# Optimization experiments

Hardware: AMD Instinct MI355X
Metric: run time of the kernel (lower is better)

## Reference

```python
import jax, jax.numpy as jnp
import numpy as np
from jax import lax

DF = 64        # forcing_size: number of teacher-forced latent dims
TF_ALPHA = 0.2 # generalized teacher forcing interpolation weight


def setup_inputs() -> dict:
    key = jax.random.key(0)
    ks = jax.random.split(key, 8)
    B, T, dx, dz, dh, S = 256, 1024, 64, 256, 1024, 16
    x_gt = jax.random.normal(ks[0], (B, T, dx), dtype=jnp.float32)
    subject = jax.random.randint(ks[1], (B,), 0, S, dtype=jnp.int32)
    obs_matrix = jax.random.normal(ks[2], (dz, dx), dtype=jnp.float32) * 0.1
    A_table = jax.random.uniform(ks[3], (S, dz), dtype=jnp.float32) * 0.9
    W1_table = jax.random.normal(ks[4], (S, dz, dh), dtype=jnp.float32) * 0.02
    W2_table = jax.random.normal(ks[5], (S, dh, dz), dtype=jnp.float32) * 0.02
    h1_table = jax.random.normal(ks[6], (S, dz), dtype=jnp.float32) * 0.02
    h2_table = jax.random.normal(ks[7], (S, dh), dtype=jnp.float32) * 0.02
    return {"x_gt": x_gt, "subject": subject, "obs_matrix": obs_matrix,
            "A_table": A_table, "W1_table": W1_table, "W2_table": W2_table,
            "h1_table": h1_table, "h2_table": h2_table}


def reference(x_gt, subject, obs_matrix, A_table, W1_table, W2_table, h1_table, h2_table):
    B, T, dx = x_gt.shape
    dz = obs_matrix.shape[0]
    # encode: x @ pinv(obs_matrix) -> (B, T, dz)
    forcing = x_gt @ jnp.linalg.pinv(obs_matrix)
    # gather per-sample parameters by subject id
    A = A_table[subject]    # (B, dz)
    W1 = W1_table[subject]  # (B, dz, dh)
    W2 = W2_table[subject]  # (B, dh, dz)
    h1 = h1_table[subject]  # (B, dz)
    h2 = h2_table[subject]  # (B, dh)

    z0 = jnp.zeros((B, dz), dtype=x_gt.dtype)
    z0 = z0.at[:, :DF].set(forcing[:, 0, :DF])

    def step(z, f_t):
        # generalized teacher forcing on first DF dims
        z = z.at[:, :DF].set(TF_ALPHA * f_t[:, :DF] + (1.0 - TF_ALPHA) * z[:, :DF])
        # vanilla shPLRNN step: A*z + W1 @ relu(W2 @ z + h2) + h1
        hidden = jax.nn.relu(jnp.einsum('bhz,bz->bh', W2, z) + h2)
        z = A * z + jnp.einsum('bzh,bh->bz', W1, hidden) + h1
        return z, z

    _, Z = lax.scan(step, z0, jnp.transpose(forcing, (1, 0, 2)))  # Z: (T, B, dz)
    # decode: (B, T, dz) @ (dz, dx)
    return jnp.transpose(Z, (1, 0, 2)) @ obs_matrix
```

## Files before the change

kernel.cpp:

```cpp
#include <hip/hip_runtime.h>


typedef _Float16 f16;
typedef _Float16 f16x8 __attribute__((ext_vector_type(8)));
typedef float f32x4 __attribute__((ext_vector_type(4)));

#define TSTEPS 1024

#define WS_C     0ul
#define WS_ZG    16384ul
#define WS_HIDG  802816ul
#define WS_ORDER 2375680ul
#define WS_CNT   2376704ul
#define WS_OFFS  2376768ul
#define WS_CTR   2376832ul
#define WS_XCC   2378880ul
#define WS_FLAG  2379392ul
#define WS_NEED  2381440ul

#define SM_ZPK   0
#define SM_ZPRE  26880
#define SM_ZSL   33792
#define SM_TBUF  39936
#define SM_AH    53760
#define SM_ORD   54016
#define SM_SIZE  54208

__device__ __forceinline__ unsigned pack2f16(float x, float y) {
    union { f16 h[2]; unsigned u; } v;
    v.h[0] = (f16)x; v.h[1] = (f16)y;
    return v.u;
}

__device__ __forceinline__ void group_barrier(int* ctr, int target,
                                              int* flg, int j, int gen,
                                              bool light) {
    __syncthreads();
    if (light) {
        if (threadIdx.x < 64) {
            if (threadIdx.x == 0)
                *(volatile int*)(flg + j) = gen;
            volatile const int* fp = (volatile const int*)(flg + (threadIdx.x & 7));
            for (;;) {
                asm volatile("buffer_inv" ::: "memory");
                int v = *fp;
                if (__all(v >= gen)) break;
                __builtin_amdgcn_s_sleep(1);
            }
            asm volatile("buffer_inv" ::: "memory");
        }
        __syncthreads();
        return;
    }
    if (threadIdx.x == 0) {
        __builtin_amdgcn_fence(__ATOMIC_RELEASE, "agent");
        __hip_atomic_fetch_add(ctr, 1, __ATOMIC_RELAXED, __HIP_MEMORY_SCOPE_AGENT);
        while (__hip_atomic_load(ctr, __ATOMIC_RELAXED, __HIP_MEMORY_SCOPE_AGENT) < target)
            __builtin_amdgcn_s_sleep(1);
        __builtin_amdgcn_fence(__ATOMIC_ACQUIRE, "agent");
    }
    __syncthreads();
}

__global__ __launch_bounds__(256) void prep_kernel(const float* __restrict__ M,
                                                   float* __restrict__ C) {
    __shared__ float aug[64 * 132];
    __shared__ float fac[64];
    int tid = threadIdx.x;
    {
        int i = tid >> 2;
        int j0 = (tid & 3) * 16;
        float acc[16];
        #pragma unroll
        for (int e = 0; e < 16; ++e) acc[e] = 0.f;
        for (int r = 0; r < 256; ++r) {
            float mi = M[r*64 + i];
            #pragma unroll
            for (int e = 0; e < 16; ++e) acc[e] += mi * M[r*64 + j0 + e];
        }
        #pragma unroll
        for (int e = 0; e < 16; ++e) aug[i*132 + j0 + e] = acc[e];
    }
    for (int idx = tid; idx < 4096; idx += 256) {
        int x = idx >> 6, c = idx & 63;
        aug[x*132 + 64 + c] = M[c*64 + x];
    }
    __syncthreads();
    for (int p = 0; p < 64; ++p) {
        float piv = aug[p*132 + p];
        __syncthreads();
        if (tid < 128) aug[p*132 + tid] /= piv;
        __syncthreads();
        if (tid < 64) fac[tid] = aug[tid*132 + p];
        __syncthreads();
        for (int idx = tid; idx < 8192; idx += 256) {
            int r = idx >> 7, c = idx & 127;
            if (r != p) aug[r*132 + c] -= fac[r] * aug[p*132 + c];
        }
        __syncthreads();
    }
    for (int idx = tid; idx < 4096; idx += 256) {
        int x = idx >> 6, c = idx & 63;
        C[x*64 + c] = aug[x*132 + 64 + c];
    }
}

__global__ __launch_bounds__(256) void forcing_kernel(const float* __restrict__ x,
        const float* __restrict__ C, float* __restrict__ fout) {
    __shared__ float xs[64 * 68];
    __shared__ float Cs[64 * 64];
    int tid = threadIdx.x;
    for (int i = tid; i < 1024; i += 256)
        ((float4*)Cs)[i] = ((const float4*)C)[i];
    long r0 = (long)blockIdx.x * 64;
    int b  = (int)(r0 >> 10);
    int t0 = (int)(r0 & 1023);
    const float4* xb = (const float4*)(x + ((long)b * 1024 + t0) * 64);
    for (int i = tid; i < 1024; i += 256) {
        float4 v = xb[i];
        int row = i >> 4, col = (i & 15) * 4;
        *(float4*)&xs[row*68 + col] = v;
    }
    __syncthreads();
    int row = tid >> 2, cg = (tid & 3) * 16;
    float acc[16];
    #pragma unroll
    for (int e = 0; e < 16; ++e) acc[e] = 0.f;
    for (int k = 0; k < 64; ++k) {
        float xv = xs[row*68 + k];
        const float* cr = &Cs[k*64 + cg];
        #pragma unroll
        for (int e = 0; e < 16; ++e) acc[e] += xv * cr[e];
    }
    float4* dst = (float4*)(fout + ((size_t)b*1024 + t0 + row)*64 + cg);
    #pragma unroll
    for (int e = 0; e < 4; ++e) {
        float4 v; v.x = acc[4*e]; v.y = acc[4*e+1]; v.z = acc[4*e+2]; v.w = acc[4*e+3];
        dst[e] = v;
    }
}

__global__ __launch_bounds__(256) void group_kernel(const int* __restrict__ subject,
        int* order, int* cnt, int* offs, int* ctr, int* flag) {
    __shared__ int lc[16], lo[16], cur[16];
    int tid = threadIdx.x;
    if (tid < 16) { lc[tid] = 0; cur[tid] = 0; }
    __syncthreads();
    int s = subject[tid];
    atomicAdd(&lc[s], 1);
    __syncthreads();
    if (tid == 0) { int a = 0; for (int i = 0; i < 16; ++i) { lo[i] = a; a += lc[i]; } }
    __syncthreads();
    int pos = lo[s] + atomicAdd(&cur[s], 1);
    order[pos] = tid;
    if (tid < 16) {
        cnt[tid] = lc[tid]; offs[tid] = lo[tid];
        ctr[tid*32] = 0;
        ctr[tid*32 + 16] = 0;
        #pragma unroll
        for (int k = 0; k < 8; ++k) flag[tid*32 + k] = 0;
    }
}

template<int NT>
__device__ __forceinline__ void run_group(int s, int j, int Bs, int off,
    const float* __restrict__ W1t, const float* __restrict__ W2t,
    const float* __restrict__ At,  const float* __restrict__ h1t,
    const float* __restrict__ h2t, const float* __restrict__ Mt,
    float* __restrict__ zg, f16* __restrict__ hidg,
    const int* __restrict__ order, int* ctr, int* flg,
    float* out, char* sm, bool light)
{
    f16*   zpk   = (f16*)(sm + SM_ZPK);
    f16*   zpre  = (f16*)(sm + SM_ZPRE);
    float* zsl   = (float*)(sm + SM_ZSL);
    f16*   tbuf  = (f16*)(sm + SM_TBUF);
    float* ah    = (float*)(sm + SM_AH);
    int*   ordl  = (int*)(sm + SM_ORD);
    float* red   = (float*)(sm + SM_ZPK);

    const int tid  = threadIdx.x;
    const int w    = tid >> 6;
    const int lane = tid & 63;
    const int q    = lane >> 4;
    const int li   = lane & 15;

    float* zgs = zg + (size_t)s * (48*256);
    char*  hgs = (char*)hidg + (size_t)s * (48*1024*2);

    if (tid < 48) ordl[tid] = (tid < Bs) ? order[off + tid] : 0;
    if (tid >= 64 && tid < 96)  ah[tid-64]      = At [s*256 + 32*j + (tid-64)];
    if (tid >= 96 && tid < 128) ah[tid-96+32]   = h1t[s*256 + 32*j + (tid-96)];
    __syncthreads();

    f16x8 w2f[2][8], w1f[2][8], mfr[8];
    float h2v[2][4];
    const f32x4 zero4 = {0.f, 0.f, 0.f, 0.f};
    #pragma unroll
    for (int m = 0; m < 2; ++m) {
        const float* src = W2t + (size_t)s*262144 + (size_t)(128*j + (2*w+m)*16 + li)*256;
        #pragma unroll
        for (int kt = 0; kt < 8; ++kt) {
            int k0 = kt*32 + q*8;
            #pragma unroll
            for (int e = 0; e < 8; ++e) w2f[m][kt][e] = (f16)src[k0+e];
        }
    }
    #pragma unroll
    for (int m = 0; m < 2; ++m) {
        const float* src = W1t + (size_t)s*262144 + (size_t)(32*j + m*16 + li)*1024;
        #pragma unroll
        for (int kt = 0; kt < 8; ++kt) {
            int k0 = (8*w + kt)*32 + q*8;
            #pragma unroll
            for (int e = 0; e < 8; ++e) w1f[m][kt][e] = (f16)src[k0+e];
        }
    }
    #pragma unroll
    for (int kt = 0; kt < 8; ++kt)
        #pragma unroll
        for (int e = 0; e < 8; ++e)
            mfr[kt][e] = (f16)Mt[(kt*32 + q*8 + e)*64 + 16*w + li];
    #pragma unroll
    for (int m = 0; m < 2; ++m)
        #pragma unroll
        for (int r = 0; r < 4; ++r)
            h2v[m][r] = h2t[s*1024 + 128*j + (2*w+m)*16 + q*4 + r];

    for (int idx = tid; idx < NT*512; idx += 256) {
        int n = idx >> 5, zdl = idx & 31;
        int zd = 32*j + zdl;
        float v = 0.f;
        if (zd < 64 && n < Bs) v = out[(size_t)ordl[n]*65536 + zd];
        zgs[n*256 + zd] = v;
    }
    int gen = 1;
    group_barrier(ctr, 8*gen, flg, j, gen, light);

    for (int t = 0; t <= TSTEPS; ++t) {
        {
            int half = tid >> 7;
            int kk = (tid & 127) * 2;
            int kl = kk - 32*j;
            #pragma unroll
            for (int i = 0; i < NT*8; ++i) {
                int n = i*2 + half;
                float zx = 0.f, zy = 0.f;
                if (n < Bs) {
                    float2 zz = *(const float2*)&zgs[n*256 + kk];
                    zx = zz.x; zy = zz.y;
                }
                float px = zx, py = zy;
                if (kk < 64) {
                    ((unsigned*)zpre)[n*36 + (kk>>1)] = pack2f16(zx, zy);
                    if (t < TSTEPS && n < Bs) {
                        float2 fv = *(const float2*)&out[((size_t)ordl[n]*1024 + t)*64 + kk];
                        px = 0.2f*fv.x + 0.8f*zx;
                        py = 0.2f*fv.y + 0.8f*zy;
                    }
                }
                ((unsigned*)zpk)[n*140 + (kk>>1)] = pack2f16(px, py);
                if (kl >= 0 && kl < 32) {
                    float2 pv; pv.x = px; pv.y = py;
                    *(float2*)&zsl[n*32 + kl] = pv;
                }
            }
        }
        __syncthreads();

        if (t > 0 && j < NT) {
            f32x4 dacc = zero4;
            #pragma unroll
            for (int kt = 0; kt < 8; ++kt) {
                f16x8 af;
                if (kt < 2) af = *(const f16x8*)&zpre[(16*j + li)*72 + kt*32 + q*8];
                else        af = *(const f16x8*)&zpk [(16*j + li)*280 + kt*32 + q*8];
                dacc = __builtin_amdgcn_mfma_f32_16x16x32_f16(af, mfr[kt], dacc, 0, 0, 0);
            }
            #pragma unroll
            for (int r = 0; r < 4; ++r) {
                int n = 16*j + q*4 + r;
                if (n < Bs)
                    out[((size_t)ordl[n]*TSTEPS + (t-1))*64 + 16*w + li] = dacc[r];
            }
        }
        if (t == TSTEPS) break;

        {
            f32x4 acc[2][NT];
            #pragma unroll
            for (int m = 0; m < 2; ++m)
                #pragma unroll
                for (int nt = 0; nt < NT; ++nt) acc[m][nt] = zero4;
            #pragma unroll
            for (int nt = 0; nt < NT; ++nt) {
                #pragma unroll
                for (int kt = 0; kt < 8; ++kt) {
                    f16x8 bf = *(const f16x8*)&zpk[(16*nt + li)*280 + kt*32 + q*8];
                    acc[0][nt] = __builtin_amdgcn_mfma_f32_16x16x32_f16(w2f[0][kt], bf, acc[0][nt], 0,0,0);
                    acc[1][nt] = __builtin_amdgcn_mfma_f32_16x16x32_f16(w2f[1][kt], bf, acc[1][nt], 0,0,0);
                }
            }
            #pragma unroll
            for (int m = 0; m < 2; ++m)
                #pragma unroll
                for (int nt = 0; nt < NT; ++nt)
                    #pragma unroll
                    for (int r = 0; r < 4; ++r) {
                        float hv = acc[m][nt][r] + h2v[m][r];
                        hv = hv > 0.f ? hv : 0.f;
                        tbuf[(nt*16 + li)*144 + (2*w+m)*16 + q*4 + r] = (f16)hv;
                    }
        }
        __syncthreads();
        for (int c = tid; c < NT*256; c += 256) {
            int n = c >> 4, cc = c & 15;
            *(f16x8*)(hgs + n*2048 + j*256 + cc*16) = *(const f16x8*)&tbuf[n*144 + cc*8];
        }
        ++gen; group_barrier(ctr, 8*gen, flg, j, gen, light);

        {
            f32x4 bacc[2][NT];
            #pragma unroll
            for (int m = 0; m < 2; ++m)
                #pragma unroll
                for (int nt = 0; nt < NT; ++nt) bacc[m][nt] = zero4;
            #pragma unroll
            for (int nt = 0; nt < NT; ++nt) {
                #pragma unroll
                for (int kt = 0; kt < 8; ++kt) {
                    f16x8 bf = *(const f16x8*)(hgs + (16*nt + li)*2048 + (8*w + kt)*64 + q*16);
                    bacc[0][nt] = __builtin_amdgcn_mfma_f32_16x16x32_f16(w1f[0][kt], bf, bacc[0][nt], 0,0,0);
                    bacc[1][nt] = __builtin_amdgcn_mfma_f32_16x16x32_f16(w1f[1][kt], bf, bacc[1][nt], 0,0,0);
                }
            }
            __syncthreads();
            #pragma unroll
            for (int m = 0; m < 2; ++m)
                #pragma unroll
                for (int nt = 0; nt < NT; ++nt)
                    *(f32x4*)&red[(size_t)((w*6 + m*3 + nt)*256 + lane*4)] = bacc[m][nt];
        }
        __syncthreads();
        for (int idx = tid; idx < NT*512; idx += 256) {
            int zdl = idx & 31, n = idx >> 5;
            int m = zdl >> 4, qq = (zdl >> 2) & 3, r = zdl & 3;
            int ln = qq*16 + (n & 15), nt = n >> 4;
            float sum = 0.f;
            #pragma unroll
            for (int ww = 0; ww < 4; ++ww)
                sum += red[(ww*6 + m*3 + nt)*256 + ln*4 + r];
            float zv = ah[zdl] * zsl[n*32 + zdl] + sum + ah[32 + zdl];
            if (n < Bs) zgs[n*256 + 32*j + zdl] = zv;
        }
        ++gen; group_barrier(ctr, 8*gen, flg, j, gen, light);
    }
}

__global__ __launch_bounds__(256, 1) void main_kernel(
    const float* W1t, const float* W2t, const float* At, const float* h1t,
    const float* h2t, const float* Mt, float* zg, f16* hidg,
    const int* order, const int* cnt, const int* offs, int* ctr, int* xccg,
    int* flag, float* out)
{
    __shared__ __align__(16) char sm[SM_SIZE];
    int bid = blockIdx.x;
    int s = (bid & 7) + 8*(bid >> 6);
    int j = (bid >> 3) & 7;
    int Bs = cnt[s];
    if (Bs <= 0) return;
    if (Bs > 48) Bs = 48;
    int off = offs[s];
    int* myctr = ctr + s*32;
    int* flg   = flag + s*32;

    int xcc;
    asm volatile("s_getreg_b32 %0, hwreg(HW_REG_XCC_ID)" : "=s"(xcc));
    xcc &= 0xf;
    if (threadIdx.x == 0) xccg[s*8 + j] = xcc;
    group_barrier(myctr + 16, 8, nullptr, 0, 0, false);
    bool light = true;
    #pragma unroll
    for (int i = 0; i < 8; ++i) light = light && (xccg[s*8 + i] == xcc);

    int NT = (Bs + 15) >> 4;
    if (NT == 1)
        run_group<1>(s, j, Bs, off, W1t, W2t, At, h1t, h2t, Mt, zg, hidg, order, myctr, flg, out, sm, light);
    else if (NT == 2)
        run_group<2>(s, j, Bs, off, W1t, W2t, At, h1t, h2t, Mt, zg, hidg, order, myctr, flg, out, sm, light);
    else
        run_group<3>(s, j, Bs, off, W1t, W2t, At, h1t, h2t, Mt, zg, hidg, order, myctr, flg, out, sm, light);
}

extern "C" void kernel_launch(void* const* d_in, const int* in_sizes, int n_in,
                              void* d_out, int out_size, void* d_ws, size_t ws_size,
                              hipStream_t stream) {
    const float* x    = (const float*)d_in[0];
    const int*   subj = (const int*)d_in[1];
    const float* Mt   = (const float*)d_in[2];
    const float* At   = (const float*)d_in[3];
    const float* W1t  = (const float*)d_in[4];
    const float* W2t  = (const float*)d_in[5];
    const float* h1t  = (const float*)d_in[6];
    const float* h2t  = (const float*)d_in[7];
    float* out = (float*)d_out;
    char*  ws  = (char*)d_ws;
    if (ws_size < WS_NEED) return;

    float* C     = (float*)(ws + WS_C);
    float* zg    = (float*)(ws + WS_ZG);
    f16*   hidg  = (f16*)(ws + WS_HIDG);
    int*   order = (int*)(ws + WS_ORDER);
    int*   cnt   = (int*)(ws + WS_CNT);
    int*   offs  = (int*)(ws + WS_OFFS);
    int*   ctr   = (int*)(ws + WS_CTR);
    int*   xccg  = (int*)(ws + WS_XCC);
    int*   flag  = (int*)(ws + WS_FLAG);

    prep_kernel<<<1, 256, 0, stream>>>(Mt, C);
    forcing_kernel<<<4096, 256, 0, stream>>>(x, C, out);
    group_kernel<<<1, 256, 0, stream>>>(subj, order, cnt, offs, ctr, flag);
    main_kernel<<<128, 256, 0, stream>>>(W1t, W2t, At, h1t, h2t, Mt,
                                         zg, hidg, order, cnt, offs, ctr, xccg,
                                         flag, out);
}
```

Measured before the change: 11.46 ms.

## Interleave two subject groups per block with split signal/wait barriers

Result: slower. 18.73 ms (+63.4%).

```diff
diff --git a/kernel.cpp b/kernel.cpp
--- a/kernel.cpp
+++ b/kernel.cpp
@@ -14,17 +14,23 @@
 #define WS_CNT   2376704ul
 #define WS_OFFS  2376768ul
 #define WS_CTR   2376832ul
-#define WS_XCC   2378880ul
-#define WS_FLAG  2379392ul
-#define WS_NEED  2381440ul
-
-#define SM_ZPK   0
-#define SM_ZPRE  26880
-#define SM_ZSL   33792
-#define SM_TBUF  39936
-#define SM_AH    53760
-#define SM_ORD   54016
-#define SM_SIZE  54208
+#define WS_GCTR  2378880ul
+#define WS_XCC   2379008ul
+#define WS_FLAG  2380032ul
+#define WS_NEED  2382080ul
+
+#define SM_ZPK_A  0
+#define SM_ZPK_B  26880
+#define SM_ZPRE_A 53760
+#define SM_ZPRE_B 60672
+#define SM_ZSL_A  67584
+#define SM_ZSL_B  70656
+#define SM_TBUF   73728
+#define SM_AH_A   80640
+#define SM_AH_B   80768
+#define SM_ORD_A  80896
+#define SM_ORD_B  81088
+#define SM_SIZE   81280
 
 __device__ __forceinline__ unsigned pack2f16(float x, float y) {
     union { f16 h[2]; unsigned u; } v;
@@ -32,15 +38,22 @@
     return v.u;
 }
 
-__device__ __forceinline__ void group_barrier(int* ctr, int target,
-                                              int* flg, int j, int gen,
-                                              bool light) {
-    __syncthreads();
+__device__ __forceinline__ void sig_flag(int* c, int* f, int jf, int gen, bool light) {
+    __syncthreads();
+    if (threadIdx.x == 0) {
+        if (light) {
+            *(volatile int*)(f + jf) = gen;
+        } else {
+            __builtin_amdgcn_fence(__ATOMIC_RELEASE, "agent");
+            __hip_atomic_fetch_add(c, 1, __ATOMIC_RELAXED, __HIP_MEMORY_SCOPE_AGENT);
+        }
+    }
+}
+
+__device__ __forceinline__ void wait_flag(int* c, int target, int* f, int gen, bool light) {
     if (light) {
         if (threadIdx.x < 64) {
-            if (threadIdx.x == 0)
-                *(volatile int*)(flg + j) = gen;
-            volatile const int* fp = (volatile const int*)(flg + (threadIdx.x & 7));
+            volatile const int* fp = (volatile const int*)(f + (threadIdx.x & 15));
             for (;;) {
                 asm volatile("buffer_inv" ::: "memory");
                 int v = *fp;
@@ -49,15 +62,12 @@
             }
             asm volatile("buffer_inv" ::: "memory");
         }
-        __syncthreads();
-        return;
-    }
-    if (threadIdx.x == 0) {
-        __builtin_amdgcn_fence(__ATOMIC_RELEASE, "agent");
-        __hip_atomic_fetch_add(ctr, 1, __ATOMIC_RELAXED, __HIP_MEMORY_SCOPE_AGENT);
-        while (__hip_atomic_load(ctr, __ATOMIC_RELAXED, __HIP_MEMORY_SCOPE_AGENT) < target)
-            __builtin_amdgcn_s_sleep(1);
-        __builtin_amdgcn_fence(__ATOMIC_ACQUIRE, "agent");
+    } else {
+        if (threadIdx.x == 0) {
+            while (__hip_atomic_load(c, __ATOMIC_RELAXED, __HIP_MEMORY_SCOPE_AGENT) < target)
+                __builtin_amdgcn_s_sleep(1);
+            __builtin_amdgcn_fence(__ATOMIC_ACQUIRE, "agent");
+        }
     }
     __syncthreads();
 }
@@ -141,7 +151,7 @@
 }
 
 __global__ __launch_bounds__(256) void group_kernel(const int* __restrict__ subject,
-        int* order, int* cnt, int* offs, int* ctr, int* flag) {
+        int* order, int* cnt, int* offs, int* ctr, int* flag, int* gctr) {
     __shared__ int lc[16], lo[16], cur[16];
     int tid = threadIdx.x;
     if (tid < 16) { lc[tid] = 0; cur[tid] = 0; }
@@ -156,28 +166,197 @@
     if (tid < 16) {
         cnt[tid] = lc[tid]; offs[tid] = lo[tid];
         ctr[tid*32] = 0;
-        ctr[tid*32 + 16] = 0;
-        #pragma unroll
-        for (int k = 0; k < 8; ++k) flag[tid*32 + k] = 0;
-    }
-}
-
-template<int NT>
-__device__ __forceinline__ void run_group(int s, int j, int Bs, int off,
+        ctr[tid*32 + 8] = 0;
+        #pragma unroll
+        for (int k = 0; k < 32; ++k) flag[tid*32 + k] = 0;
+    }
+    if (tid == 0) gctr[0] = 0;
+}
+
+template<int NT>
+__device__ __forceinline__ void stage_subj(int t, int jX, int Bs, const int* ordl,
+    const float* zgs, f16* zpk, f16* zpre, float* zsl, const float* out)
+{
+    int tid = threadIdx.x;
+    int half = tid >> 7;
+    int kk = (tid & 127) * 2;
+    int kl = kk - 16*jX;
+    #pragma unroll
+    for (int i = 0; i < NT*8; ++i) {
+        int n = i*2 + half;
+        float zx = 0.f, zy = 0.f;
+        if (n < Bs) {
+            float2 zz = *(const float2*)&zgs[n*256 + kk];
+            zx = zz.x; zy = zz.y;
+        }
+        float px = zx, py = zy;
+        if (kk < 64) {
+            ((unsigned*)zpre)[n*36 + (kk>>1)] = pack2f16(zx, zy);
+            if (t < TSTEPS && n < Bs) {
+                float2 fv = *(const float2*)&out[((size_t)ordl[n]*1024 + t)*64 + kk];
+                px = 0.2f*fv.x + 0.8f*zx;
+                py = 0.2f*fv.y + 0.8f*zy;
+            }
+        }
+        ((unsigned*)zpk)[n*140 + (kk>>1)] = pack2f16(px, py);
+        if (kl >= 0 && kl < 16) {
+            float2 pv; pv.x = px; pv.y = py;
+            *(float2*)&zsl[n*16 + kl] = pv;
+        }
+    }
+}
+
+template<int NT>
+__device__ __forceinline__ void phaseA_subj(const f16x8 (&w2f)[8], const float (&h2v)[4],
+    const f16* zpk, f16* tbuf, int w, int q, int li)
+{
+    const f32x4 zero4 = {0.f, 0.f, 0.f, 0.f};
+    f32x4 acc[NT];
+    #pragma unroll
+    for (int nt = 0; nt < NT; ++nt) acc[nt] = zero4;
+    #pragma unroll
+    for (int nt = 0; nt < NT; ++nt)
+        #pragma unroll
+        for (int kt = 0; kt < 8; ++kt) {
+            f16x8 bf = *(const f16x8*)&zpk[(16*nt + li)*280 + kt*32 + q*8];
+            acc[nt] = __builtin_amdgcn_mfma_f32_16x16x32_f16(w2f[kt], bf, acc[nt], 0,0,0);
+        }
+    #pragma unroll
+    for (int nt = 0; nt < NT; ++nt)
+        #pragma unroll
+        for (int r = 0; r < 4; ++r) {
+            float hv = acc[nt][r] + h2v[r];
+            hv = hv > 0.f ? hv : 0.f;
+            tbuf[(nt*16 + li)*72 + 16*w + 4*q + r] = (f16)hv;
+        }
+}
+
+template<int NT>
+__device__ __forceinline__ void hidg_store(int jX, const f16* tbuf, char* hgs) {
+    for (int c = threadIdx.x; c < NT*128; c += 256) {
+        int n = c >> 3, cc = c & 7;
+        *(f16x8*)(hgs + n*2048 + jX*128 + cc*16) = *(const f16x8*)&tbuf[n*72 + cc*8];
+    }
+}
+
+template<int NT>
+__device__ __forceinline__ void decode_subj(int t, int jX, int Bs, const int* ordl,
+    const f16* zpk, const f16* zpre, const f16x8 (&mfr)[8], float* out,
+    int w, int q, int li)
+{
+    const f32x4 zero4 = {0.f, 0.f, 0.f, 0.f};
+    f32x4 dacc = zero4;
+    #pragma unroll
+    for (int kt = 0; kt < 8; ++kt) {
+        f16x8 af;
+        if (kt < 2) af = *(const f16x8*)&zpre[(16*jX + li)*72 + kt*32 + q*8];
+        else        af = *(const f16x8*)&zpk [(16*jX + li)*280 + kt*32 + q*8];
+        dacc = __builtin_amdgcn_mfma_f32_16x16x32_f16(af, mfr[kt], dacc, 0, 0, 0);
+    }
+    #pragma unroll
+    for (int r = 0; r < 4; ++r) {
+        int n = 16*jX + q*4 + r;
+        if (n < Bs)
+            out[((size_t)ordl[n]*TSTEPS + (t-1))*64 + 16*w + li] = dacc[r];
+    }
+}
+
+template<int NT>
+__device__ __forceinline__ void phaseB_subj(const f16x8 (&w1f)[8], const char* hgs,
+    float* red, int w, int q, int li, int lane)
+{
+    const f32x4 zero4 = {0.f, 0.f, 0.f, 0.f};
+    f32x4 bacc[NT];
+    #pragma unroll
+    for (int nt = 0; nt < NT; ++nt) bacc[nt] = zero4;
+    #pragma unroll
+    for (int nt = 0; nt < NT; ++nt)
+        #pragma unroll
+        for (int kt = 0; kt < 8; ++kt) {
+            f16x8 bf = *(const f16x8*)(hgs + (16*nt + li)*2048 + (8*w + kt)*64 + q*16);
+            bacc[nt] = __builtin_amdgcn_mfma_f32_16x16x32_f16(w1f[kt], bf, bacc[nt], 0,0,0);
+        }
+    __syncthreads();
+    #pragma unroll
+    for (int nt = 0; nt < NT; ++nt)
+        *(f32x4*)&red[(size_t)((w*NT + nt)*256 + lane*4)] = bacc[nt];
+}
+
+template<int NT>
+__device__ __forceinline__ void reduce_subj(int jX, int Bs, const float* red,
+    const float* zsl, const float* ah, float* zgs)
+{
+    for (int idx = threadIdx.x; idx < NT*256; idx += 256) {
+        int n = idx >> 4, zdl = idx & 15;
+        int qq = zdl >> 2, r = zdl & 3;
+        int ln = qq*16 + (n & 15), nt = n >> 4;
+        float sum = 0.f;
+        #pragma unroll
+        for (int ww = 0; ww < 4; ++ww)
+            sum += red[(ww*NT + nt)*256 + ln*4 + r];
+        float zv = ah[zdl] * zsl[n*16 + zdl] + sum + ah[16 + zdl];
+        if (n < Bs) zgs[n*256 + 16*jX + zdl] = zv;
+    }
+}
+
+template<int NT>
+__device__ __forceinline__ void init_z0(int jX, int Bs, const int* ordl,
+    const float* out, float* zgs)
+{
+    for (int idx = threadIdx.x; idx < NT*256; idx += 256) {
+        int n = idx >> 4, zdl = idx & 15;
+        int zd = 16*jX + zdl;
+        float v = 0.f;
+        if (zd < 64 && n < Bs) v = out[(size_t)ordl[n]*65536 + zd];
+        zgs[n*256 + zd] = v;
+    }
+}
+
+__device__ __forceinline__ void load_weights(int s, int jX,
+    const float* W1t, const float* W2t, const float* h2t,
+    f16x8 (&w2f)[8], f16x8 (&w1f)[8], float (&h2v)[4], int w, int q, int li)
+{
+    const float* src2 = W2t + (size_t)s*262144 + (size_t)(64*jX + 16*w + li)*256;
+    #pragma unroll
+    for (int kt = 0; kt < 8; ++kt) {
+        int k0 = kt*32 + q*8;
+        #pragma unroll
+        for (int e = 0; e < 8; ++e) w2f[kt][e] = (f16)src2[k0+e];
+    }
+    const float* src1 = W1t + (size_t)s*262144 + (size_t)(16*jX + li)*1024 + 256*w;
+    #pragma unroll
+    for (int kt = 0; kt < 8; ++kt) {
+        int k0 = kt*32 + q*8;
+        #pragma unroll
+        for (int e = 0; e < 8; ++e) w1f[kt][e] = (f16)src1[k0+e];
+    }
+    #pragma unroll
+    for (int r = 0; r < 4; ++r)
+        h2v[r] = h2t[s*1024 + 64*jX + 16*w + q*4 + r];
+}
+
+template<int NTA, int NTB>
+__device__ void run_pair(
+    int sA, int jA, int BsA, int offA, bool doA, bool lightA,
+    int sB, int jB, int BsB, int offB, bool doB, bool lightB,
     const float* __restrict__ W1t, const float* __restrict__ W2t,
     const float* __restrict__ At,  const float* __restrict__ h1t,
     const float* __restrict__ h2t, const float* __restrict__ Mt,
     float* __restrict__ zg, f16* __restrict__ hidg,
-    const int* __restrict__ order, int* ctr, int* flg,
-    float* out, char* sm, bool light)
-{
-    f16*   zpk   = (f16*)(sm + SM_ZPK);
-    f16*   zpre  = (f16*)(sm + SM_ZPRE);
-    float* zsl   = (float*)(sm + SM_ZSL);
+    const int* __restrict__ order, int* ctr, int* flag, float* out, char* sm)
+{
+    f16*   zpkA  = (f16*)(sm + SM_ZPK_A);
+    f16*   zpkB  = (f16*)(sm + SM_ZPK_B);
+    f16*   zpreA = (f16*)(sm + SM_ZPRE_A);
+    f16*   zpreB = (f16*)(sm + SM_ZPRE_B);
+    float* zslA  = (float*)(sm + SM_ZSL_A);
+    float* zslB  = (float*)(sm + SM_ZSL_B);
     f16*   tbuf  = (f16*)(sm + SM_TBUF);
-    float* ah    = (float*)(sm + SM_AH);
-    int*   ordl  = (int*)(sm + SM_ORD);
-    float* red   = (float*)(sm + SM_ZPK);
+    float* ahA   = (float*)(sm + SM_AH_A);
+    float* ahB   = (float*)(sm + SM_AH_B);
+    int*   ordlA = (int*)(sm + SM_ORD_A);
+    int*   ordlB = (int*)(sm + SM_ORD_B);
+    float* red   = (float*)(sm + SM_ZPK_A);
 
     const int tid  = threadIdx.x;
     const int w    = tid >> 6;
@@ -185,211 +364,138 @@
     const int q    = lane >> 4;
     const int li   = lane & 15;
 
-    float* zgs = zg + (size_t)s * (48*256);
-    char*  hgs = (char*)hidg + (size_t)s * (48*1024*2);
-
-    if (tid < 48) ordl[tid] = (tid < Bs) ? order[off + tid] : 0;
-    if (tid >= 64 && tid < 96)  ah[tid-64]      = At [s*256 + 32*j + (tid-64)];
-    if (tid >= 96 && tid < 128) ah[tid-96+32]   = h1t[s*256 + 32*j + (tid-96)];
-    __syncthreads();
-
-    f16x8 w2f[2][8], w1f[2][8], mfr[8];
-    float h2v[2][4];
-    const f32x4 zero4 = {0.f, 0.f, 0.f, 0.f};
-    #pragma unroll
-    for (int m = 0; m < 2; ++m) {
-        const float* src = W2t + (size_t)s*262144 + (size_t)(128*j + (2*w+m)*16 + li)*256;
-        #pragma unroll
-        for (int kt = 0; kt < 8; ++kt) {
-            int k0 = kt*32 + q*8;
-            #pragma unroll
-            for (int e = 0; e < 8; ++e) w2f[m][kt][e] = (f16)src[k0+e];
-        }
-    }
-    #pragma unroll
-    for (int m = 0; m < 2; ++m) {
-        const float* src = W1t + (size_t)s*262144 + (size_t)(32*j + m*16 + li)*1024;
-        #pragma unroll
-        for (int kt = 0; kt < 8; ++kt) {
-            int k0 = (8*w + kt)*32 + q*8;
-            #pragma unroll
-            for (int e = 0; e < 8; ++e) w1f[m][kt][e] = (f16)src[k0+e];
-        }
-    }
+    float* zgsA = zg + (size_t)sA * (48*256);
+    float* zgsB = zg + (size_t)sB * (48*256);
+    char*  hgsA = (char*)hidg + (size_t)sA * 98304;
+    char*  hgsB = (char*)hidg + (size_t)sB * 98304;
+    int* c1A = ctr + sA*32;      int* c2A = ctr + sA*32 + 8;
+    int* c1B = ctr + sB*32;      int* c2B = ctr + sB*32 + 8;
+    int* f1A = flag + sA*32;     int* f2A = flag + sA*32 + 16;
+    int* f1B = flag + sB*32;     int* f2B = flag + sB*32 + 16;
+
+    if (tid < 48)                 ordlA[tid]    = (doA && tid < BsA) ? order[offA + tid] : 0;
+    else if (tid < 96)            ordlB[tid-48] = (doB && (tid-48) < BsB) ? order[offB + tid-48] : 0;
+    if (tid >= 128 && tid < 144)  ahA[tid-128]      = At [sA*256 + 16*jA + (tid-128)];
+    if (tid >= 144 && tid < 160)  ahA[16 + tid-144] = h1t[sA*256 + 16*jA + (tid-144)];
+    if (tid >= 160 && tid < 176)  ahB[tid-160]      = At [sB*256 + 16*jB + (tid-160)];
+    if (tid >= 176 && tid < 192)  ahB[16 + tid-176] = h1t[sB*256 + 16*jB + (tid-176)];
+    __syncthreads();
+
+    f16x8 w2fA[8], w1fA[8], w2fB[8], w1fB[8], mfr[8];
+    float h2vA[4], h2vB[4];
+    load_weights(sA, jA, W1t, W2t, h2t, w2fA, w1fA, h2vA, w, q, li);
+    load_weights(sB, jB, W1t, W2t, h2t, w2fB, w1fB, h2vB, w, q, li);
     #pragma unroll
     for (int kt = 0; kt < 8; ++kt)
         #pragma unroll
         for (int e = 0; e < 8; ++e)
             mfr[kt][e] = (f16)Mt[(kt*32 + q*8 + e)*64 + 16*w + li];
-    #pragma unroll
-    for (int m = 0; m < 2; ++m)
-        #pragma unroll
-        for (int r = 0; r < 4; ++r)
-            h2v[m][r] = h2t[s*1024 + 128*j + (2*w+m)*16 + q*4 + r];
-
-    for (int idx = tid; idx < NT*512; idx += 256) {
-        int n = idx >> 5, zdl = idx & 31;
-        int zd = 32*j + zdl;
-        float v = 0.f;
-        if (zd < 64 && n < Bs) v = out[(size_t)ordl[n]*65536 + zd];
-        zgs[n*256 + zd] = v;
-    }
-    int gen = 1;
-    group_barrier(ctr, 8*gen, flg, j, gen, light);
-
-    for (int t = 0; t <= TSTEPS; ++t) {
-        {
-            int half = tid >> 7;
-            int kk = (tid & 127) * 2;
-            int kl = kk - 32*j;
-            #pragma unroll
-            for (int i = 0; i < NT*8; ++i) {
-                int n = i*2 + half;
-                float zx = 0.f, zy = 0.f;
-                if (n < Bs) {
-                    float2 zz = *(const float2*)&zgs[n*256 + kk];
-                    zx = zz.x; zy = zz.y;
-                }
-                float px = zx, py = zy;
-                if (kk < 64) {
-                    ((unsigned*)zpre)[n*36 + (kk>>1)] = pack2f16(zx, zy);
-                    if (t < TSTEPS && n < Bs) {
-                        float2 fv = *(const float2*)&out[((size_t)ordl[n]*1024 + t)*64 + kk];
-                        px = 0.2f*fv.x + 0.8f*zx;
-                        py = 0.2f*fv.y + 0.8f*zy;
-                    }
-                }
-                ((unsigned*)zpk)[n*140 + (kk>>1)] = pack2f16(px, py);
-                if (kl >= 0 && kl < 32) {
-                    float2 pv; pv.x = px; pv.y = py;
-                    *(float2*)&zsl[n*32 + kl] = pv;
-                }
-            }
-        }
+
+    if (doA) { init_z0<NTA>(jA, BsA, ordlA, out, zgsA); sig_flag(c2A, f2A, jA, 1, lightA); }
+    if (doB) { init_z0<NTB>(jB, BsB, ordlB, out, zgsB); sig_flag(c2B, f2B, jB, 1, lightB); }
+
+    for (int t = 0; t < TSTEPS; ++t) {
+        if (doA) {
+            wait_flag(c2A, 16*(t+1), f2A, t+1, lightA);
+            stage_subj<NTA>(t, jA, BsA, ordlA, zgsA, zpkA, zpreA, zslA, out);
+            __syncthreads();
+            phaseA_subj<NTA>(w2fA, h2vA, zpkA, tbuf, w, q, li);
+            __syncthreads();
+            hidg_store<NTA>(jA, tbuf, hgsA);
+            sig_flag(c1A, f1A, jA, t+1, lightA);
+        }
+        if (doB) {
+            wait_flag(c2B, 16*(t+1), f2B, t+1, lightB);
+            stage_subj<NTB>(t, jB, BsB, ordlB, zgsB, zpkB, zpreB, zslB, out);
+            __syncthreads();
+            phaseA_subj<NTB>(w2fB, h2vB, zpkB, tbuf, w, q, li);
+            __syncthreads();
+            hidg_store<NTB>(jB, tbuf, hgsB);
+            sig_flag(c1B, f1B, jB, t+1, lightB);
+        }
+        if (doA && t > 0 && jA < NTA)
+            decode_subj<NTA>(t, jA, BsA, ordlA, zpkA, zpreA, mfr, out, w, q, li);
+        if (doA) {
+            wait_flag(c1A, 16*(t+1), f1A, t+1, lightA);
+            phaseB_subj<NTA>(w1fA, hgsA, red, w, q, li, lane);
+            __syncthreads();
+            reduce_subj<NTA>(jA, BsA, red, zslA, ahA, zgsA);
+            sig_flag(c2A, f2A, jA, t+2, lightA);
+        }
+        if (doB) {
+            wait_flag(c1B, 16*(t+1), f1B, t+1, lightB);
+            phaseB_subj<NTB>(w1fB, hgsB, red, w, q, li, lane);
+            __syncthreads();
+            reduce_subj<NTB>(jB, BsB, red, zslB, ahB, zgsB);
+            sig_flag(c2B, f2B, jB, t+2, lightB);
+        }
+    }
+    if (doA && jA < NTA) {
+        wait_flag(c2A, 16*(TSTEPS+1), f2A, TSTEPS+1, lightA);
+        stage_subj<NTA>(TSTEPS, jA, BsA, ordlA, zgsA, zpkA, zpreA, zslA, out);
         __syncthreads();
-
-        if (t > 0 && j < NT) {
-            f32x4 dacc = zero4;
-            #pragma unroll
-            for (int kt = 0; kt < 8; ++kt) {
-                f16x8 af;
-                if (kt < 2) af = *(const f16x8*)&zpre[(16*j + li)*72 + kt*32 + q*8];
-                else        af = *(const f16x8*)&zpk [(16*j + li)*280 + kt*32 + q*8];
-                dacc = __builtin_amdgcn_mfma_f32_16x16x32_f16(af, mfr[kt], dacc, 0, 0, 0);
-            }
-            #pragma unroll
-            for (int r = 0; r < 4; ++r) {
-                int n = 16*j + q*4 + r;
-                if (n < Bs)
-                    out[((size_t)ordl[n]*TSTEPS + (t-1))*64 + 16*w + li] = dacc[r];
-            }
-        }
-        if (t == TSTEPS) break;
-
-        {
-            f32x4 acc[2][NT];
-            #pragma unroll
-            for (int m = 0; m < 2; ++m)
-                #pragma unroll
-                for (int nt = 0; nt < NT; ++nt) acc[m][nt] = zero4;
-            #pragma unroll
-            for (int nt = 0; nt < NT; ++nt) {
-                #pragma unroll
-                for (int kt = 0; kt < 8; ++kt) {
-                    f16x8 bf = *(const f16x8*)&zpk[(16*nt + li)*280 + kt*32 + q*8];
-                    acc[0][nt] = __builtin_amdgcn_mfma_f32_16x16x32_f16(w2f[0][kt], bf, acc[0][nt], 0,0,0);
-                    acc[1][nt] = __builtin_amdgcn_mfma_f32_16x16x32_f16(w2f[1][kt], bf, acc[1][nt], 0,0,0);
-                }
-            }
-            #pragma unroll
-            for (int m = 0; m < 2; ++m)
-                #pragma unroll
-                for (int nt = 0; nt < NT; ++nt)
-                    #pragma unroll
-                    for (int r = 0; r < 4; ++r) {
-                        float hv = acc[m][nt][r] + h2v[m][r];
-                        hv = hv > 0.f ? hv : 0.f;
-                        tbuf[(nt*16 + li)*144 + (2*w+m)*16 + q*4 + r] = (f16)hv;
-                    }
-        }
-        __syncthreads();
-        for (int c = tid; c < NT*256; c += 256) {
-            int n = c >> 4, cc = c & 15;
-            *(f16x8*)(hgs + n*2048 + j*256 + cc*16) = *(const f16x8*)&tbuf[n*144 + cc*8];
-        }
-        ++gen; group_barrier(ctr, 8*gen, flg, j, gen, light);
-
-        {
-            f32x4 bacc[2][NT];
-            #pragma unroll
-            for (int m = 0; m < 2; ++m)
-                #pragma unroll
-                for (int nt = 0; nt < NT; ++nt) bacc[m][nt] = zero4;
-            #pragma unroll
-            for (int nt = 0; nt < NT; ++nt) {
-                #pragma unroll
-                for (int kt = 0; kt < 8; ++kt) {
-                    f16x8 bf = *(const f16x8*)(hgs + (16*nt + li)*2048 + (8*w + kt)*64 + q*16);
-                    bacc[0][nt] = __builtin_amdgcn_mfma_f32_16x16x32_f16(w1f[0][kt], bf, bacc[0][nt], 0,0,0);
-                    bacc[1][nt] = __builtin_amdgcn_mfma_f32_16x16x32_f16(w1f[1][kt], bf, bacc[1][nt], 0,0,0);
-                }
-            }
-            __syncthreads();
-            #pragma unroll
-            for (int m = 0; m < 2; ++m)
-                #pragma unroll
-                for (int nt = 0; nt < NT; ++nt)
-                    *(f32x4*)&red[(size_t)((w*6 + m*3 + nt)*256 + lane*4)] = bacc[m][nt];
-        }
-        __syncthreads();
-        for (int idx = tid; idx < NT*512; idx += 256) {
-            int zdl = idx & 31, n = idx >> 5;
-            int m = zdl >> 4, qq = (zdl >> 2) & 3, r = zdl & 3;
-            int ln = qq*16 + (n & 15), nt = n >> 4;
-            float sum = 0.f;
-            #pragma unroll
-            for (int ww = 0; ww < 4; ++ww)
-                sum += red[(ww*6 + m*3 + nt)*256 + ln*4 + r];
-            float zv = ah[zdl] * zsl[n*32 + zdl] + sum + ah[32 + zdl];
-            if (n < Bs) zgs[n*256 + 32*j + zdl] = zv;
-        }
-        ++gen; group_barrier(ctr, 8*gen, flg, j, gen, light);
+        decode_subj<NTA>(TSTEPS, jA, BsA, ordlA, zpkA, zpreA, mfr, out, w, q, li);
     }
 }
 
 __global__ __launch_bounds__(256, 1) void main_kernel(
     const float* W1t, const float* W2t, const float* At, const float* h1t,
     const float* h2t, const float* Mt, float* zg, f16* hidg,
-    const int* order, const int* cnt, const int* offs, int* ctr, int* xccg,
-    int* flag, float* out)
+    const int* order, const int* cnt, const int* offs, int* ctr, int* gctr,
+    int* xccg, int* flag, float* out)
 {
     __shared__ __align__(16) char sm[SM_SIZE];
     int bid = blockIdx.x;
-    int s = (bid & 7) + 8*(bid >> 6);
-    int j = (bid >> 3) & 7;
-    int Bs = cnt[s];
-    if (Bs <= 0) return;
-    if (Bs > 48) Bs = 48;
-    int off = offs[s];
-    int* myctr = ctr + s*32;
-    int* flg   = flag + s*32;
+    int sA = bid & 15, jA = bid >> 4;
+    int sB = sA ^ 8,   jB = 8 + jA;
 
     int xcc;
     asm volatile("s_getreg_b32 %0, hwreg(HW_REG_XCC_ID)" : "=s"(xcc));
     xcc &= 0xf;
-    if (threadIdx.x == 0) xccg[s*8 + j] = xcc;
-    group_barrier(myctr + 16, 8, nullptr, 0, 0, false);
-    bool light = true;
-    #pragma unroll
-    for (int i = 0; i < 8; ++i) light = light && (xccg[s*8 + i] == xcc);
-
-    int NT = (Bs + 15) >> 4;
-    if (NT == 1)
-        run_group<1>(s, j, Bs, off, W1t, W2t, At, h1t, h2t, Mt, zg, hidg, order, myctr, flg, out, sm, light);
-    else if (NT == 2)
-        run_group<2>(s, j, Bs, off, W1t, W2t, At, h1t, h2t, Mt, zg, hidg, order, myctr, flg, out, sm, light);
-    else
-        run_group<3>(s, j, Bs, off, W1t, W2t, At, h1t, h2t, Mt, zg, hidg, order, myctr, flg, out, sm, light);
+    if (threadIdx.x == 0) { xccg[sA*16 + jA] = xcc; xccg[sB*16 + jB] = xcc; }
+    __syncthreads();
+    if (threadIdx.x == 0) {
+        __builtin_amdgcn_fence(__ATOMIC_RELEASE, "agent");
+        __hip_atomic_fetch_add(gctr, 1, __ATOMIC_RELAXED, __HIP_MEMORY_SCOPE_AGENT);
+        while (__hip_atomic_load(gctr, __ATOMIC_RELAXED, __HIP_MEMORY_SCOPE_AGENT) < 128)
+            __builtin_amdgcn_s_sleep(1);
+        __builtin_amdgcn_fence(__ATOMIC_ACQUIRE, "agent");
+    }
+    __syncthreads();
+    bool lightA = true, lightB = true;
+    for (int i = 0; i < 16; ++i) {
+        lightA = lightA && (xccg[sA*16 + i] == xcc);
+        lightB = lightB && (xccg[sB*16 + i] == xcc);
+    }
+
+    int BsA = cnt[sA]; if (BsA > 48) BsA = 48;
+    int BsB = cnt[sB]; if (BsB > 48) BsB = 48;
+    bool doA = BsA > 0, doB = BsB > 0;
+    if (!doA && !doB) return;
+    int NTA = doA ? ((BsA + 15) >> 4) : 1;
+    int NTB = doB ? ((BsB + 15) >> 4) : 1;
+    int offA = offs[sA], offB = offs[sB];
+
+    switch ((NTA-1)*3 + (NTB-1)) {
+    case 0: run_pair<1,1>(sA,jA,BsA,offA,doA,lightA, sB,jB,BsB,offB,doB,lightB,
+            W1t,W2t,At,h1t,h2t,Mt,zg,hidg,order,ctr,flag,out,sm); break;
+    case 1: run_pair<1,2>(sA,jA,BsA,offA,doA,lightA, sB,jB,BsB,offB,doB,lightB,
+            W1t,W2t,At,h1t,h2t,Mt,zg,hidg,order,ctr,flag,out,sm); break;
+    case 2: run_pair<1,3>(sA,jA,BsA,offA,doA,lightA, sB,jB,BsB,offB,doB,lightB,
+            W1t,W2t,At,h1t,h2t,Mt,zg,hidg,order,ctr,flag,out,sm); break;
+    case 3: run_pair<2,1>(sA,jA,BsA,offA,doA,lightA, sB,jB,BsB,offB,doB,lightB,
+            W1t,W2t,At,h1t,h2t,Mt,zg,hidg,order,ctr,flag,out,sm); break;
+    case 4: run_pair<2,2>(sA,jA,BsA,offA,doA,lightA, sB,jB,BsB,offB,doB,lightB,
+            W1t,W2t,At,h1t,h2t,Mt,zg,hidg,order,ctr,flag,out,sm); break;
+    case 5: run_pair<2,3>(sA,jA,BsA,offA,doA,lightA, sB,jB,BsB,offB,doB,lightB,
+            W1t,W2t,At,h1t,h2t,Mt,zg,hidg,order,ctr,flag,out,sm); break;
+    case 6: run_pair<3,1>(sA,jA,BsA,offA,doA,lightA, sB,jB,BsB,offB,doB,lightB,
+            W1t,W2t,At,h1t,h2t,Mt,zg,hidg,order,ctr,flag,out,sm); break;
+    case 7: run_pair<3,2>(sA,jA,BsA,offA,doA,lightA, sB,jB,BsB,offB,doB,lightB,
+            W1t,W2t,At,h1t,h2t,Mt,zg,hidg,order,ctr,flag,out,sm); break;
+    default: run_pair<3,3>(sA,jA,BsA,offA,doA,lightA, sB,jB,BsB,offB,doB,lightB,
+            W1t,W2t,At,h1t,h2t,Mt,zg,hidg,order,ctr,flag,out,sm); break;
+    }
 }
 
 extern "C" void kernel_launch(void* const* d_in, const int* in_sizes, int n_in,
@@ -414,13 +520,14 @@
     int*   cnt   = (int*)(ws + WS_CNT);
     int*   offs  = (int*)(ws + WS_OFFS);
     int*   ctr   = (int*)(ws + WS_CTR);
+    int*   gctr  = (int*)(ws + WS_GCTR);
     int*   xccg  = (int*)(ws + WS_XCC);
     int*   flag  = (int*)(ws + WS_FLAG);
 
     prep_kernel<<<1, 256, 0, stream>>>(Mt, C);
     forcing_kernel<<<4096, 256, 0, stream>>>(x, C, out);
-    group_kernel<<<1, 256, 0, stream>>>(subj, order, cnt, offs, ctr, flag);
+    group_kernel<<<1, 256, 0, stream>>>(subj, order, cnt, offs, ctr, flag, gctr);
     main_kernel<<<128, 256, 0, stream>>>(W1t, W2t, At, h1t, h2t, Mt,
-                                         zg, hidg, order, cnt, offs, ctr, xccg,
-                                         flag, out);
-}
+                                         zg, hidg, order, cnt, offs, ctr, gctr,
+                                         xccg, flag, out);
+}
```
